# Optimization experiments

Hardware: AMD Instinct MI355X
Metric: run time of the kernel (lower is better)

Reference implementation:

```python
import jax, jax.numpy as jnp
import numpy as np

B, L, D, H = 2, 2048, 1024, 16
HD = D // H
RECENCY_BIAS = 0.1
EPS = 1e-8


def setup_inputs() -> dict:
    key = jax.random.key(0)
    k1, k2, k3, k4 = jax.random.split(key, 4)
    x = jax.random.normal(k1, (B, L, D), dtype=jnp.float32)
    # positive time gaps in [0, 10)
    time_diffs = jax.random.uniform(k2, (B, L, L), dtype=jnp.float32) * 10.0
    # packed qkv in-projection, as in nn.MultiheadAttention
    in_proj_w = jax.random.normal(k3, (3 * D, D), dtype=jnp.float32) * (D ** -0.5)
    in_proj_b = jax.random.normal(k4, (3 * D,), dtype=jnp.float32) * 0.01
    return {"x": x, "time_diffs": time_diffs, "in_proj_w": in_proj_w, "in_proj_b": in_proj_b}


def reference(x, time_diffs, in_proj_w, in_proj_b):
    # packed in-projection (q,k,v from same x, self-attention)
    qkv = x @ in_proj_w.T + in_proj_b              # [B, L, 3D]
    q, k, v = jnp.split(qkv, 3, axis=-1)
    # split heads: [B, H, L, HD]
    def heads(t):
        return t.reshape(B, L, H, HD).transpose(0, 2, 1, 3)
    q, k, v = heads(q), heads(k), heads(v)
    scores = jnp.einsum("bhqd,bhkd->bhqk", q, k) * (HD ** -0.5)
    w = jax.nn.softmax(scores, axis=-1)            # [B, H, L, L]
    # MultiheadAttention returns head-averaged weights (average_attn_weights=True)
    attn_weights = jnp.mean(w, axis=1)             # [B, L, L]
    # temporal decay reweight + renormalize
    decay = jnp.exp(-RECENCY_BIAS * time_diffs)
    attn_weights = attn_weights * decay
    attn_weights = attn_weights / (jnp.sum(attn_weights, axis=-1, keepdims=True) + EPS)
    # weighted sum against raw x (bypasses learned V / out_proj)
    output = jnp.einsum("bqk,bkd->bqd", attn_weights, x)
    return output, attn_weights
```

## Files before the change

### kernel.cpp

```cpp
#include <hip/hip_runtime.h>
#include <hip/hip_bf16.h>
#include <math.h>

namespace {
constexpr int kB = 2;
constexpr int kL = 2048;
constexpr int kD = 1024;
constexpr int kH = 16;
constexpr int kHD = 64;
constexpr float kScale = 0.125f;
constexpr float kRecency = 0.1f;
constexpr float kEps = 1e-8f;

constexpr size_t kN4 = 4194304;
}

typedef __bf16 bf16x8 __attribute__((ext_vector_type(8)));
typedef float f32x4 __attribute__((ext_vector_type(4)));
typedef unsigned short u16;
typedef u16 u16x8 __attribute__((ext_vector_type(8)));

__device__ inline u16 f2bf(float v) {
  unsigned int u = __float_as_uint(v);
  unsigned int r = (u + 0x7FFFu + ((u >> 16) & 1u)) >> 16;
  return (u16)r;
}
__device__ inline float bf2f(u16 u) { return __uint_as_float((unsigned int)u << 16); }

__global__ __launch_bounds__(256) void k_cvt_xw(const float* __restrict__ x,
                                                const float* __restrict__ w,
                                                u16* __restrict__ xh, u16* __restrict__ xl,
                                                u16* __restrict__ wh, u16* __restrict__ wl) {
  const size_t id = (size_t)blockIdx.x * 256 + threadIdx.x;
  const bool isx = id < 1048576;
  const float4 v = isx ? reinterpret_cast<const float4*>(x)[id]
                       : reinterpret_cast<const float4*>(w)[id - 1048576];
  const float vv[4] = {v.x, v.y, v.z, v.w};
  ushort4 h4, l4;
#pragma unroll
  for (int c = 0; c < 4; ++c) {
    const u16 hu = f2bf(vv[c]);
    ((u16*)&h4)[c] = hu;
    ((u16*)&l4)[c] = f2bf(vv[c] - bf2f(hu));
  }
  const size_t o = (isx ? id : id - 1048576) * 4;
  if (isx) {
    *reinterpret_cast<ushort4*>(xh + o) = h4;
    *reinterpret_cast<ushort4*>(xl + o) = l4;
  } else {
    *reinterpret_cast<ushort4*>(wh + o) = h4;
    *reinterpret_cast<ushort4*>(wl + o) = l4;
  }
}

__global__ __launch_bounds__(256, 2) void k_qkproj(const u16* __restrict__ xh, const u16* __restrict__ xl,
                                                   const u16* __restrict__ wh, const u16* __restrict__ wl,
                                                   const float* __restrict__ bias,
                                                   u16* __restrict__ qhi, u16* __restrict__ qlo,
                                                   u16* __restrict__ khi, u16* __restrict__ klo) {
  __shared__ u16 Ah[8192], Al[8192], Bh[8192], Bl[8192];
  const int tid = threadIdx.x;
  const int wave = tid >> 6, lane = tid & 63;
  const int wr = wave >> 1, wc = wave & 1;
  const int n0 = blockIdx.x * 128;
  const int m0 = blockIdx.y * 128;
  f32x4 acc[4][4] = {};
  for (int k0 = 0; k0 < kD; k0 += 64) {
    __syncthreads();
#pragma unroll
    for (int c2 = 0; c2 < 4; ++c2) {
      const int chunk = tid + c2 * 256;
      const int idx = chunk >> 3, cc = chunk & 7;
      const int lo = (((idx >> 4) * 8 + cc) * 16 + (idx & 15)) * 8;
      const size_t gw = (size_t)(n0 + idx) * kD + k0 + cc * 8;
      const size_t gx = (size_t)(m0 + idx) * kD + k0 + cc * 8;
      *reinterpret_cast<u16x8*>(&Ah[lo]) = *reinterpret_cast<const u16x8*>(wh + gw);
      *reinterpret_cast<u16x8*>(&Al[lo]) = *reinterpret_cast<const u16x8*>(wl + gw);
      *reinterpret_cast<u16x8*>(&Bh[lo]) = *reinterpret_cast<const u16x8*>(xh + gx);
      *reinterpret_cast<u16x8*>(&Bl[lo]) = *reinterpret_cast<const u16x8*>(xl + gx);
    }
    __syncthreads();
#pragma unroll
    for (int w = 0; w < 2; ++w) {
      const int kc = w * 4 + (lane >> 4);
      bf16x8 Afh[4], Afl[4], Bfh[4], Bfl[4];
#pragma unroll
      for (int i = 0; i < 4; ++i) {
        const int la = (((wr * 4 + i) * 8 + kc) * 16 + (lane & 15)) * 8;
        const int lb = (((wc * 4 + i) * 8 + kc) * 16 + (lane & 15)) * 8;
        Afh[i] = *reinterpret_cast<const bf16x8*>(&Ah[la]);
        Afl[i] = *reinterpret_cast<const bf16x8*>(&Al[la]);
        Bfh[i] = *reinterpret_cast<const bf16x8*>(&Bh[lb]);
        Bfl[i] = *reinterpret_cast<const bf16x8*>(&Bl[lb]);
      }
#pragma unroll
      for (int i = 0; i < 4; ++i)
#pragma unroll
        for (int j = 0; j < 4; ++j) {
          acc[i][j] = __builtin_amdgcn_mfma_f32_16x16x32_bf16(Afh[i], Bfh[j], acc[i][j], 0, 0, 0);
          acc[i][j] = __builtin_amdgcn_mfma_f32_16x16x32_bf16(Afh[i], Bfl[j], acc[i][j], 0, 0, 0);
          acc[i][j] = __builtin_amdgcn_mfma_f32_16x16x32_bf16(Afl[i], Bfh[j], acc[i][j], 0, 0, 0);
        }
    }
  }
  const int hglob = (n0 + wr * 64) >> 6;
  const bool isq = hglob < 16;
  const int hh = hglob & 15;
  u16* __restrict__ dh = isq ? qhi : khi;
  u16* __restrict__ dl = isq ? qlo : klo;
#pragma unroll
  for (int i = 0; i < 4; ++i) {
    const int hd0 = i * 16 + ((lane >> 4) << 2);
    const f32x4 b4 = *reinterpret_cast<const f32x4*>(bias + n0 + wr * 64 + hd0);
#pragma unroll
    for (int j = 0; j < 4; ++j) {
      const int m = m0 + wc * 64 + j * 16 + (lane & 15);
      const int bb = m >> 11, ll = m & (kL - 1);
      ushort4 vh, vl;
#pragma unroll
      for (int r = 0; r < 4; ++r) {
        const float v = acc[i][j][r] + b4[r];
        const u16 hu = f2bf(v);
        ((u16*)&vh)[r] = hu;
        ((u16*)&vl)[r] = f2bf(v - bf2f(hu));
      }
      const size_t o = (((size_t)bb * kH + hh) * kL + ll) * kHD + hd0;
      *reinterpret_cast<ushort4*>(dh + o) = vh;
      *reinterpret_cast<ushort4*>(dl + o) = vl;
    }
  }
}

__global__ __launch_bounds__(256) void k_stats(const u16* __restrict__ qh, const u16* __restrict__ ql,
                                               const u16* __restrict__ kh, const u16* __restrict__ kl,
                                               float* __restrict__ mo, float* __restrict__ ilo) {
  __shared__ u16 Kh[4096];
  __shared__ u16 Kl[4096];
  const int tid = threadIdx.x;
  const int wave = tid >> 6, lane = tid & 63;
  const int qt = blockIdx.x;
  const int bh = blockIdx.y;
  const size_t base = (size_t)bh * kL * kHD;
  const int row0 = qt * 64 + wave * 16;
  const size_t qoff = base + (size_t)(row0 + (lane & 15)) * kHD + (lane >> 4) * 8;
  const bf16x8 aqh0 = *reinterpret_cast<const bf16x8*>(qh + qoff);
  const bf16x8 aqh1 = *reinterpret_cast<const bf16x8*>(qh + qoff + 32);
  const bf16x8 aql0 = *reinterpret_cast<const bf16x8*>(ql + qoff);
  const bf16x8 aql1 = *reinterpret_cast<const bf16x8*>(ql + qoff + 32);
  float m[4], l[4];
#pragma unroll
  for (int r = 0; r < 4; ++r) { m[r] = -INFINITY; l[r] = 0.f; }
  for (int kt = 0; kt < kL; kt += 64) {
    __syncthreads();
#pragma unroll
    for (int c = tid; c < 512; c += 256) {
      const int col = c >> 3, cc = c & 7;
      const size_t g = base + (size_t)(kt + col) * kHD + cc * 8;
      const int lo = ((((col >> 4) * 2 + (cc >> 2)) * 4 + (cc & 3)) * 16 + (col & 15)) * 8;
      *reinterpret_cast<u16x8*>(&Kh[lo]) = *reinterpret_cast<const u16x8*>(kh + g);
      *reinterpret_cast<u16x8*>(&Kl[lo]) = *reinterpret_cast<const u16x8*>(kl + g);
    }
    __syncthreads();
#pragma unroll
    for (int cs = 0; cs < 4; ++cs) {
      const int f0 = (((cs * 2 + 0) * 4 + (lane >> 4)) * 16 + (lane & 15)) * 8;
      const int f1 = (((cs * 2 + 1) * 4 + (lane >> 4)) * 16 + (lane & 15)) * 8;
      const bf16x8 bh0 = *reinterpret_cast<const bf16x8*>(&Kh[f0]);
      const bf16x8 bh1 = *reinterpret_cast<const bf16x8*>(&Kh[f1]);
      const bf16x8 bl0 = *reinterpret_cast<const bf16x8*>(&Kl[f0]);
      const bf16x8 bl1 = *reinterpret_cast<const bf16x8*>(&Kl[f1]);
      f32x4 s = {0.f, 0.f, 0.f, 0.f};
      s = __builtin_amdgcn_mfma_f32_16x16x32_bf16(aqh0, bh0, s, 0, 0, 0);
      s = __builtin_amdgcn_mfma_f32_16x16x32_bf16(aqh1, bh1, s, 0, 0, 0);
      s = __builtin_amdgcn_mfma_f32_16x16x32_bf16(aqh0, bl0, s, 0, 0, 0);
      s = __builtin_amdgcn_mfma_f32_16x16x32_bf16(aqh1, bl1, s, 0, 0, 0);
      s = __builtin_amdgcn_mfma_f32_16x16x32_bf16(aql0, bh0, s, 0, 0, 0);
      s = __builtin_amdgcn_mfma_f32_16x16x32_bf16(aql1, bh1, s, 0, 0, 0);
#pragma unroll
      for (int r = 0; r < 4; ++r) {
        const float sc = s[r] * kScale;
        const float nm = fmaxf(m[r], sc);
        l[r] = l[r] * __expf(m[r] - nm) + __expf(sc - nm);
        m[r] = nm;
      }
    }
  }
#pragma unroll
  for (int r = 0; r < 4; ++r) {
#pragma unroll
    for (int off = 1; off < 16; off <<= 1) {
      const float mo2 = __shfl_xor(m[r], off);
      const float lo2 = __shfl_xor(l[r], off);
      const float nm = fmaxf(m[r], mo2);
      l[r] = l[r] * __expf(m[r] - nm) + lo2 * __expf(mo2 - nm);
      m[r] = nm;
    }
  }
  if ((lane & 15) == 0) {
#pragma unroll
    for (int r = 0; r < 4; ++r) {
      const int row = row0 + (lane >> 4) * 4 + r;
      mo[(size_t)bh * kL + row] = m[r];
      ilo[(size_t)bh * kL + row] = 1.0f / l[r];
    }
  }
}

__global__ __launch_bounds__(256) void k_attn(const u16* __restrict__ qh, const u16* __restrict__ ql,
                                              const u16* __restrict__ kh, const u16* __restrict__ kl,
                                              const float* __restrict__ ms, const float* __restrict__ ils,
                                              const float* __restrict__ td,
                                              float* __restrict__ attn, float* __restrict__ rowsum) {
  __shared__ u16 Kh[8192];
  __shared__ u16 Kl[8192];
  __shared__ float msS[16][64];
  __shared__ float ilS[16][64];
  const int tid = threadIdx.x;
  const int wave = tid >> 6, lane = tid & 63;
  const int kb = blockIdx.x;
  const int qb = blockIdx.y;
  const int b = blockIdx.z;
#pragma unroll
  for (int c = tid; c < 1024; c += 256) {
    const int h = c >> 6, r = c & 63;
    msS[h][r] = ms[((size_t)b * kH + h) * kL + qb * 64 + r];
    ilS[h][r] = ils[((size_t)b * kH + h) * kL + qb * 64 + r];
  }
  const int row0 = qb * 64 + wave * 16;
  float wacc[8][4] = {};
  for (int h = 0; h < kH; ++h) {
    const size_t base = ((size_t)b * kH + h) * kL * kHD;
    __syncthreads();
#pragma unroll
    for (int c = tid; c < 1024; c += 256) {
      const int col = c >> 3, cc = c & 7;
      const size_t g = base + (size_t)(kb * 128 + col) * kHD + cc * 8;
      const int lo = ((((col >> 4) * 2 + (cc >> 2)) * 4 + (cc & 3)) * 16 + (col & 15)) * 8;
      *reinterpret_cast<u16x8*>(&Kh[lo]) = *reinterpret_cast<const u16x8*>(kh + g);
      *reinterpret_cast<u16x8*>(&Kl[lo]) = *reinterpret_cast<const u16x8*>(kl + g);
    }
    __syncthreads();
    const size_t qoff = base + (size_t)(row0 + (lane & 15)) * kHD + (lane >> 4) * 8;
    const bf16x8 aqh0 = *reinterpret_cast<const bf16x8*>(qh + qoff);
    const bf16x8 aqh1 = *reinterpret_cast<const bf16x8*>(qh + qoff + 32);
    const bf16x8 aql0 = *reinterpret_cast<const bf16x8*>(ql + qoff);
    const bf16x8 aql1 = *reinterpret_cast<const bf16x8*>(ql + qoff + 32);
    const f32x4 mrow = *reinterpret_cast<const f32x4*>(&msS[h][wave * 16 + (lane >> 4) * 4]);
    const f32x4 irow = *reinterpret_cast<const f32x4*>(&ilS[h][wave * 16 + (lane >> 4) * 4]);
#pragma unroll
    for (int cs = 0; cs < 8; ++cs) {
      const int f0 = (((cs * 2 + 0) * 4 + (lane >> 4)) * 16 + (lane & 15)) * 8;
      const int f1 = (((cs * 2 + 1) * 4 + (lane >> 4)) * 16 + (lane & 15)) * 8;
      const bf16x8 bkh0 = *reinterpret_cast<const bf16x8*>(&Kh[f0]);
      const bf16x8 bkh1 = *reinterpret_cast<const bf16x8*>(&Kh[f1]);
      const bf16x8 bkl0 = *reinterpret_cast<const bf16x8*>(&Kl[f0]);
      const bf16x8 bkl1 = *reinterpret_cast<const bf16x8*>(&Kl[f1]);
      f32x4 s = {0.f, 0.f, 0.f, 0.f};
      s = __builtin_amdgcn_mfma_f32_16x16x32_bf16(aqh0, bkh0, s, 0, 0, 0);
      s = __builtin_amdgcn_mfma_f32_16x16x32_bf16(aqh1, bkh1, s, 0, 0, 0);
      s = __builtin_amdgcn_mfma_f32_16x16x32_bf16(aqh0, bkl0, s, 0, 0, 0);
      s = __builtin_amdgcn_mfma_f32_16x16x32_bf16(aqh1, bkl1, s, 0, 0, 0);
      s = __builtin_amdgcn_mfma_f32_16x16x32_bf16(aql0, bkh0, s, 0, 0, 0);
      s = __builtin_amdgcn_mfma_f32_16x16x32_bf16(aql1, bkh1, s, 0, 0, 0);
#pragma unroll
      for (int r = 0; r < 4; ++r)
        wacc[cs][r] += __expf(fmaf(s[r], kScale, -mrow[r])) * irow[r];
    }
  }
  const float invH = 1.0f / kH;
#pragma unroll
  for (int r = 0; r < 4; ++r) {
    const int row = row0 + (lane >> 4) * 4 + r;
    float rs = 0.f;
#pragma unroll
    for (int cs = 0; cs < 8; ++cs) {
      const int col = kb * 128 + cs * 16 + (lane & 15);
      const size_t idx = ((size_t)b * kL + row) * kL + col;
      const float o = wacc[cs][r] * invH * __expf(-kRecency * td[idx]);
      attn[idx] = o;
      rs += o;
    }
#pragma unroll
    for (int off = 1; off < 16; off <<= 1) rs += __shfl_xor(rs, off);
    if ((lane & 15) == 0) atomicAdd(&rowsum[(size_t)b * kL + row], rs);
  }
}

__global__ __launch_bounds__(256) void k_norm(float* __restrict__ attn,
                                              const float* __restrict__ rowsum,
                                              u16* __restrict__ abf) {
  const int row = blockIdx.x;
  const float inv = 1.0f / (rowsum[row] + kEps);
  float* p = attn + (size_t)row * kL;
  u16* q = abf + (size_t)row * kL;
  const int i0 = threadIdx.x * 8;
  float4 a = *reinterpret_cast<float4*>(p + i0);
  float4 b = *reinterpret_cast<float4*>(p + i0 + 4);
  a.x *= inv; a.y *= inv; a.z *= inv; a.w *= inv;
  b.x *= inv; b.y *= inv; b.z *= inv; b.w *= inv;
  *reinterpret_cast<float4*>(p + i0) = a;
  *reinterpret_cast<float4*>(p + i0 + 4) = b;
  u16x8 h;
  h[0] = f2bf(a.x); h[1] = f2bf(a.y); h[2] = f2bf(a.z); h[3] = f2bf(a.w);
  h[4] = f2bf(b.x); h[5] = f2bf(b.y); h[6] = f2bf(b.z); h[7] = f2bf(b.w);
  *reinterpret_cast<u16x8*>(q + i0) = h;
}

__global__ __launch_bounds__(256) void k_cvt_xT(const float* __restrict__ x,
                                                u16* __restrict__ xth, u16* __restrict__ xtl) {
  __shared__ u16 Th[64][72];
  __shared__ u16 Tl[64][72];
  const int tid = threadIdx.x;
  const int l0 = blockIdx.x * 64, d0 = blockIdx.y * 64, b = blockIdx.z;
#pragma unroll
  for (int rep = 0; rep < 4; ++rep) {
    const int lr = (tid >> 4) + rep * 16;
    const int dc = (tid & 15) * 4;
    const float4 v = *reinterpret_cast<const float4*>(x + ((size_t)b * kL + l0 + lr) * kD + d0 + dc);
    const float vv[4] = {v.x, v.y, v.z, v.w};
#pragma unroll
    for (int c = 0; c < 4; ++c) {
      const u16 hu = f2bf(vv[c]);
      Th[dc + c][lr] = hu;
      Tl[dc + c][lr] = f2bf(vv[c] - bf2f(hu));
    }
  }
  __syncthreads();
#pragma unroll
  for (int rep = 0; rep < 2; ++rep) {
    const int chunk = tid + rep * 256;
    const int dd = chunk >> 3, part = chunk & 7;
    const size_t o = ((size_t)b * kD + d0 + dd) * kL + l0 + part * 8;
    *reinterpret_cast<u16x8*>(xth + o) = *reinterpret_cast<const u16x8*>(&Th[dd][part * 8]);
    *reinterpret_cast<u16x8*>(xtl + o) = *reinterpret_cast<const u16x8*>(&Tl[dd][part * 8]);
  }
}

__global__ __launch_bounds__(256, 2) void k_out(const u16* __restrict__ abf,
                                                const u16* __restrict__ xth, const u16* __restrict__ xtl,
                                                float* __restrict__ out) {
  __shared__ u16 Ah[8192], Bh[8192], Bl[8192];
  const int tid = threadIdx.x;
  const int wave = tid >> 6, lane = tid & 63;
  const int wr = wave >> 1, wc = wave & 1;
  const int m0 = blockIdx.x * 128;
  const int n0 = blockIdx.y * 128;
  const int b = blockIdx.z;
  f32x4 acc[4][4] = {};
  for (int k0 = 0; k0 < kL; k0 += 64) {
    __syncthreads();
#pragma unroll
    for (int c2 = 0; c2 < 4; ++c2) {
      const int chunk = tid + c2 * 256;
      const int idx = chunk >> 3, cc = chunk & 7;
      const int lo = (((idx >> 4) * 8 + cc) * 16 + (idx & 15)) * 8;
      const size_t ga = ((size_t)b * kL + m0 + idx) * kL + k0 + cc * 8;
      const size_t gb = ((size_t)b * kD + n0 + idx) * kL + k0 + cc * 8;
      *reinterpret_cast<u16x8*>(&Ah[lo]) = *reinterpret_cast<const u16x8*>(abf + ga);
      *reinterpret_cast<u16x8*>(&Bh[lo]) = *reinterpret_cast<const u16x8*>(xth + gb);
      *reinterpret_cast<u16x8*>(&Bl[lo]) = *reinterpret_cast<const u16x8*>(xtl + gb);
    }
    __syncthreads();
#pragma unroll
    for (int w = 0; w < 2; ++w) {
      const int kc = w * 4 + (lane >> 4);
      bf16x8 Afh[4], Bfh[4], Bfl[4];
#pragma unroll
      for (int i = 0; i < 4; ++i) {
        const int la = (((wr * 4 + i) * 8 + kc) * 16 + (lane & 15)) * 8;
        const int lb = (((wc * 4 + i) * 8 + kc) * 16 + (lane & 15)) * 8;
        Afh[i] = *reinterpret_cast<const bf16x8*>(&Ah[la]);
        Bfh[i] = *reinterpret_cast<const bf16x8*>(&Bh[lb]);
        Bfl[i] = *reinterpret_cast<const bf16x8*>(&Bl[lb]);
      }
#pragma unroll
      for (int i = 0; i < 4; ++i)
#pragma unroll
        for (int j = 0; j < 4; ++j) {
          acc[i][j] = __builtin_amdgcn_mfma_f32_16x16x32_bf16(Afh[i], Bfh[j], acc[i][j], 0, 0, 0);
          acc[i][j] = __builtin_amdgcn_mfma_f32_16x16x32_bf16(Afh[i], Bfl[j], acc[i][j], 0, 0, 0);
        }
    }
  }
#pragma unroll
  for (int i = 0; i < 4; ++i) {
    const int row = m0 + wr * 64 + i * 16 + ((lane >> 4) << 2);
#pragma unroll
    for (int j = 0; j < 4; ++j) {
      const int col = n0 + wc * 64 + j * 16 + (lane & 15);
#pragma unroll
      for (int r = 0; r < 4; ++r)
        out[((size_t)b * kL + row + r) * kD + col] = acc[i][j][r];
    }
  }
}

extern "C" void kernel_launch(void* const* d_in, const int* in_sizes, int n_in,
                              void* d_out, int out_size, void* d_ws, size_t ws_size,
                              hipStream_t stream) {
  (void)in_sizes; (void)n_in; (void)out_size; (void)ws_size;
  const float* x = (const float*)d_in[0];
  const float* td = (const float*)d_in[1];
  const float* w = (const float*)d_in[2];
  const float* bias = (const float*)d_in[3];
  float* out = (float*)d_out;
  float* attn = out + (size_t)kB * kL * kD;

  u16* base = (u16*)d_ws;
  u16* qhi = base;
  u16* qlo = base + kN4;
  u16* khi = base + 2 * kN4;
  u16* klo = base + 3 * kN4;
  u16* xah = base + 4 * kN4;
  u16* xal = base + 5 * kN4;
  u16* attn_bf = xah;
  u16* xth = qhi;
  u16* xtl = qlo;
  u16* whi = base + 6 * kN4;
  u16* wlo = whi + 2097152;
  float* fb = (float*)(wlo + 2097152);
  float* mb = fb;
  float* ilb = fb + 65536;
  float* rsb = fb + 131072;

  hipLaunchKernelGGL(k_cvt_xw, dim3(6144), dim3(256), 0, stream, x, w, xah, xal, whi, wlo);
  hipLaunchKernelGGL(k_qkproj, dim3(16, 32), dim3(256), 0, stream, xah, xal, whi, wlo, bias,
                     qhi, qlo, khi, klo);
  hipLaunchKernelGGL(k_stats, dim3(32, 32), dim3(256), 0, stream, qhi, qlo, khi, klo, mb, ilb);
  hipMemsetAsync(rsb, 0, (size_t)kB * kL * sizeof(float), stream);
  hipLaunchKernelGGL(k_attn, dim3(16, 32, 2), dim3(256), 0, stream, qhi, qlo, khi, klo, mb, ilb,
                     td, attn, rsb);
  hipLaunchKernelGGL(k_norm, dim3(kB * kL), dim3(256), 0, stream, attn, rsb, attn_bf);
  hipLaunchKernelGGL(k_cvt_xT, dim3(32, 16, 2), dim3(256), 0, stream, x, xth, xtl);
  hipLaunchKernelGGL(k_out, dim3(16, 8, 2), dim3(256), 0, stream, attn_bf, xth, xtl, out);
}
```

Before: 507.1 us.

## Switch split-precision MFMA from bf16 to fp16 and drop online max in softmax stats

Replaces bf16 hi/lo split arithmetic with fp16, which has more mantissa bits, so fewer correction MFMAs are needed: two instead of three in the projection, and four instead of six in the score GEMMs. The x low part and the K low part are no longer produced at all. Q is prescaled by scale*log2e so softmax can use exp2, and the online max is dropped: the stats kernel sums exp2 directly, with a fixed -4 offset folding in the head average, and the attn kernel uses one log-normalizer. LDS layouts get a padded stride to reduce bank conflicts, and the stats kernel reads K straight from global memory. Without the max subtraction, exp2 can overflow or lose accuracy if scores are large, and fp16 range limits may affect accuracy.

```diff
diff --git a/kernel.cpp b/kernel.cpp
--- a/kernel.cpp
+++ b/kernel.cpp
@@ -8,57 +8,50 @@
 constexpr int kD = 1024;
 constexpr int kH = 16;
 constexpr int kHD = 64;
-constexpr float kScale = 0.125f;
-constexpr float kRecency = 0.1f;
+constexpr float kQScale = 0.125f * 1.44269504088896340736f;
+constexpr float kDecay2 = -0.1f * 1.44269504088896340736f;
 constexpr float kEps = 1e-8f;
-
 constexpr size_t kN4 = 4194304;
 }
 
-typedef __bf16 bf16x8 __attribute__((ext_vector_type(8)));
+typedef _Float16 f16;
+typedef f16 f16x4 __attribute__((ext_vector_type(4)));
+typedef f16 f16x8 __attribute__((ext_vector_type(8)));
 typedef float f32x4 __attribute__((ext_vector_type(4)));
-typedef unsigned short u16;
-typedef u16 u16x8 __attribute__((ext_vector_type(8)));
-
-__device__ inline u16 f2bf(float v) {
-  unsigned int u = __float_as_uint(v);
-  unsigned int r = (u + 0x7FFFu + ((u >> 16) & 1u)) >> 16;
-  return (u16)r;
-}
-__device__ inline float bf2f(u16 u) { return __uint_as_float((unsigned int)u << 16); }
 
 __global__ __launch_bounds__(256) void k_cvt_xw(const float* __restrict__ x,
                                                 const float* __restrict__ w,
-                                                u16* __restrict__ xh, u16* __restrict__ xl,
-                                                u16* __restrict__ wh, u16* __restrict__ wl) {
+                                                f16* __restrict__ xh,
+                                                f16* __restrict__ wh, f16* __restrict__ wl) {
   const size_t id = (size_t)blockIdx.x * 256 + threadIdx.x;
-  const bool isx = id < 1048576;
-  const float4 v = isx ? reinterpret_cast<const float4*>(x)[id]
-                       : reinterpret_cast<const float4*>(w)[id - 1048576];
-  const float vv[4] = {v.x, v.y, v.z, v.w};
-  ushort4 h4, l4;
-#pragma unroll
-  for (int c = 0; c < 4; ++c) {
-    const u16 hu = f2bf(vv[c]);
-    ((u16*)&h4)[c] = hu;
-    ((u16*)&l4)[c] = f2bf(vv[c] - bf2f(hu));
-  }
-  const size_t o = (isx ? id : id - 1048576) * 4;
-  if (isx) {
-    *reinterpret_cast<ushort4*>(xh + o) = h4;
-    *reinterpret_cast<ushort4*>(xl + o) = l4;
+  if (id < 1048576) {
+    const float4 v = reinterpret_cast<const float4*>(x)[id];
+    const float vv[4] = {v.x, v.y, v.z, v.w};
+    f16x4 h;
+#pragma unroll
+    for (int c = 0; c < 4; ++c) h[c] = (f16)vv[c];
+    *reinterpret_cast<f16x4*>(xh + id * 4) = h;
   } else {
-    *reinterpret_cast<ushort4*>(wh + o) = h4;
-    *reinterpret_cast<ushort4*>(wl + o) = l4;
-  }
-}
-
-__global__ __launch_bounds__(256, 2) void k_qkproj(const u16* __restrict__ xh, const u16* __restrict__ xl,
-                                                   const u16* __restrict__ wh, const u16* __restrict__ wl,
+    const size_t id2 = id - 1048576;
+    const float4 v = reinterpret_cast<const float4*>(w)[id2];
+    const float vv[4] = {v.x, v.y, v.z, v.w};
+    f16x4 h, l;
+#pragma unroll
+    for (int c = 0; c < 4; ++c) {
+      h[c] = (f16)vv[c];
+      l[c] = (f16)(vv[c] - (float)h[c]);
+    }
+    *reinterpret_cast<f16x4*>(wh + id2 * 4) = h;
+    *reinterpret_cast<f16x4*>(wl + id2 * 4) = l;
+  }
+}
+
+__global__ __launch_bounds__(256, 2) void k_qkproj(const f16* __restrict__ xh,
+                                                   const f16* __restrict__ wh, const f16* __restrict__ wl,
                                                    const float* __restrict__ bias,
-                                                   u16* __restrict__ qhi, u16* __restrict__ qlo,
-                                                   u16* __restrict__ khi, u16* __restrict__ klo) {
-  __shared__ u16 Ah[8192], Al[8192], Bh[8192], Bl[8192];
+                                                   f16* __restrict__ qhi, f16* __restrict__ qlo,
+                                                   f16* __restrict__ khi) {
+  __shared__ f16 Ah[8704], Al[8704], Bh[8704];
   const int tid = threadIdx.x;
   const int wave = tid >> 6, lane = tid & 63;
   const int wr = wave >> 1, wc = wave & 1;
@@ -71,43 +64,38 @@
     for (int c2 = 0; c2 < 4; ++c2) {
       const int chunk = tid + c2 * 256;
       const int idx = chunk >> 3, cc = chunk & 7;
-      const int lo = (((idx >> 4) * 8 + cc) * 16 + (idx & 15)) * 8;
+      const int lo = ((idx >> 4) * 8 + cc) * 136 + (idx & 15) * 8;
       const size_t gw = (size_t)(n0 + idx) * kD + k0 + cc * 8;
       const size_t gx = (size_t)(m0 + idx) * kD + k0 + cc * 8;
-      *reinterpret_cast<u16x8*>(&Ah[lo]) = *reinterpret_cast<const u16x8*>(wh + gw);
-      *reinterpret_cast<u16x8*>(&Al[lo]) = *reinterpret_cast<const u16x8*>(wl + gw);
-      *reinterpret_cast<u16x8*>(&Bh[lo]) = *reinterpret_cast<const u16x8*>(xh + gx);
-      *reinterpret_cast<u16x8*>(&Bl[lo]) = *reinterpret_cast<const u16x8*>(xl + gx);
-    }
-    __syncthreads();
-#pragma unroll
-    for (int w = 0; w < 2; ++w) {
-      const int kc = w * 4 + (lane >> 4);
-      bf16x8 Afh[4], Afl[4], Bfh[4], Bfl[4];
+      *reinterpret_cast<f16x8*>(&Ah[lo]) = *reinterpret_cast<const f16x8*>(wh + gw);
+      *reinterpret_cast<f16x8*>(&Al[lo]) = *reinterpret_cast<const f16x8*>(wl + gw);
+      *reinterpret_cast<f16x8*>(&Bh[lo]) = *reinterpret_cast<const f16x8*>(xh + gx);
+    }
+    __syncthreads();
+#pragma unroll
+    for (int z = 0; z < 2; ++z) {
+      const int kc = z * 4 + (lane >> 4);
+      f16x8 Afh[4], Afl[4], Bfh[4];
 #pragma unroll
       for (int i = 0; i < 4; ++i) {
-        const int la = (((wr * 4 + i) * 8 + kc) * 16 + (lane & 15)) * 8;
-        const int lb = (((wc * 4 + i) * 8 + kc) * 16 + (lane & 15)) * 8;
-        Afh[i] = *reinterpret_cast<const bf16x8*>(&Ah[la]);
-        Afl[i] = *reinterpret_cast<const bf16x8*>(&Al[la]);
-        Bfh[i] = *reinterpret_cast<const bf16x8*>(&Bh[lb]);
-        Bfl[i] = *reinterpret_cast<const bf16x8*>(&Bl[lb]);
+        const int la = ((wr * 4 + i) * 8 + kc) * 136 + (lane & 15) * 8;
+        const int lb = ((wc * 4 + i) * 8 + kc) * 136 + (lane & 15) * 8;
+        Afh[i] = *reinterpret_cast<const f16x8*>(&Ah[la]);
+        Afl[i] = *reinterpret_cast<const f16x8*>(&Al[la]);
+        Bfh[i] = *reinterpret_cast<const f16x8*>(&Bh[lb]);
       }
 #pragma unroll
       for (int i = 0; i < 4; ++i)
 #pragma unroll
         for (int j = 0; j < 4; ++j) {
-          acc[i][j] = __builtin_amdgcn_mfma_f32_16x16x32_bf16(Afh[i], Bfh[j], acc[i][j], 0, 0, 0);
-          acc[i][j] = __builtin_amdgcn_mfma_f32_16x16x32_bf16(Afh[i], Bfl[j], acc[i][j], 0, 0, 0);
-          acc[i][j] = __builtin_amdgcn_mfma_f32_16x16x32_bf16(Afl[i], Bfh[j], acc[i][j], 0, 0, 0);
+          acc[i][j] = __builtin_amdgcn_mfma_f32_16x16x32_f16(Afh[i], Bfh[j], acc[i][j], 0, 0, 0);
+          acc[i][j] = __builtin_amdgcn_mfma_f32_16x16x32_f16(Afl[i], Bfh[j], acc[i][j], 0, 0, 0);
         }
     }
   }
   const int hglob = (n0 + wr * 64) >> 6;
   const bool isq = hglob < 16;
   const int hh = hglob & 15;
-  u16* __restrict__ dh = isq ? qhi : khi;
-  u16* __restrict__ dl = isq ? qlo : klo;
 #pragma unroll
   for (int i = 0; i < 4; ++i) {
     const int hd0 = i * 16 + ((lane >> 4) << 2);
@@ -116,26 +104,30 @@
     for (int j = 0; j < 4; ++j) {
       const int m = m0 + wc * 64 + j * 16 + (lane & 15);
       const int bb = m >> 11, ll = m & (kL - 1);
-      ushort4 vh, vl;
-#pragma unroll
-      for (int r = 0; r < 4; ++r) {
-        const float v = acc[i][j][r] + b4[r];
-        const u16 hu = f2bf(v);
-        ((u16*)&vh)[r] = hu;
-        ((u16*)&vl)[r] = f2bf(v - bf2f(hu));
+      const size_t o = (((size_t)bb * kH + hh) * kL + ll) * kHD + hd0;
+      if (isq) {
+        f16x4 vh, vl;
+#pragma unroll
+        for (int r = 0; r < 4; ++r) {
+          const float v = (acc[i][j][r] + b4[r]) * kQScale;
+          vh[r] = (f16)v;
+          vl[r] = (f16)(v - (float)vh[r]);
+        }
+        *reinterpret_cast<f16x4*>(qhi + o) = vh;
+        *reinterpret_cast<f16x4*>(qlo + o) = vl;
+      } else {
+        f16x4 vh;
+#pragma unroll
+        for (int r = 0; r < 4; ++r) vh[r] = (f16)(acc[i][j][r] + b4[r]);
+        *reinterpret_cast<f16x4*>(khi + o) = vh;
       }
-      const size_t o = (((size_t)bb * kH + hh) * kL + ll) * kHD + hd0;
-      *reinterpret_cast<ushort4*>(dh + o) = vh;
-      *reinterpret_cast<ushort4*>(dl + o) = vl;
-    }
-  }
-}
-
-__global__ __launch_bounds__(256) void k_stats(const u16* __restrict__ qh, const u16* __restrict__ ql,
-                                               const u16* __restrict__ kh, const u16* __restrict__ kl,
-                                               float* __restrict__ mo, float* __restrict__ ilo) {
-  __shared__ u16 Kh[4096];
-  __shared__ u16 Kl[4096];
+    }
+  }
+}
+
+__global__ __launch_bounds__(256) void k_stats(const f16* __restrict__ qh, const f16* __restrict__ ql,
+                                               const f16* __restrict__ kh,
+                                               float* __restrict__ nlo) {
   const int tid = threadIdx.x;
   const int wave = tid >> 6, lane = tid & 63;
   const int qt = blockIdx.x;
@@ -143,131 +135,86 @@
   const size_t base = (size_t)bh * kL * kHD;
   const int row0 = qt * 64 + wave * 16;
   const size_t qoff = base + (size_t)(row0 + (lane & 15)) * kHD + (lane >> 4) * 8;
-  const bf16x8 aqh0 = *reinterpret_cast<const bf16x8*>(qh + qoff);
-  const bf16x8 aqh1 = *reinterpret_cast<const bf16x8*>(qh + qoff + 32);
-  const bf16x8 aql0 = *reinterpret_cast<const bf16x8*>(ql + qoff);
-  const bf16x8 aql1 = *reinterpret_cast<const bf16x8*>(ql + qoff + 32);
-  float m[4], l[4];
-#pragma unroll
-  for (int r = 0; r < 4; ++r) { m[r] = -INFINITY; l[r] = 0.f; }
-  for (int kt = 0; kt < kL; kt += 64) {
-    __syncthreads();
-#pragma unroll
-    for (int c = tid; c < 512; c += 256) {
-      const int col = c >> 3, cc = c & 7;
-      const size_t g = base + (size_t)(kt + col) * kHD + cc * 8;
-      const int lo = ((((col >> 4) * 2 + (cc >> 2)) * 4 + (cc & 3)) * 16 + (col & 15)) * 8;
-      *reinterpret_cast<u16x8*>(&Kh[lo]) = *reinterpret_cast<const u16x8*>(kh + g);
-      *reinterpret_cast<u16x8*>(&Kl[lo]) = *reinterpret_cast<const u16x8*>(kl + g);
-    }
-    __syncthreads();
-#pragma unroll
-    for (int cs = 0; cs < 4; ++cs) {
-      const int f0 = (((cs * 2 + 0) * 4 + (lane >> 4)) * 16 + (lane & 15)) * 8;
-      const int f1 = (((cs * 2 + 1) * 4 + (lane >> 4)) * 16 + (lane & 15)) * 8;
-      const bf16x8 bh0 = *reinterpret_cast<const bf16x8*>(&Kh[f0]);
-      const bf16x8 bh1 = *reinterpret_cast<const bf16x8*>(&Kh[f1]);
-      const bf16x8 bl0 = *reinterpret_cast<const bf16x8*>(&Kl[f0]);
-      const bf16x8 bl1 = *reinterpret_cast<const bf16x8*>(&Kl[f1]);
-      f32x4 s = {0.f, 0.f, 0.f, 0.f};
-      s = __builtin_amdgcn_mfma_f32_16x16x32_bf16(aqh0, bh0, s, 0, 0, 0);
-      s = __builtin_amdgcn_mfma_f32_16x16x32_bf16(aqh1, bh1, s, 0, 0, 0);
-      s = __builtin_amdgcn_mfma_f32_16x16x32_bf16(aqh0, bl0, s, 0, 0, 0);
-      s = __builtin_amdgcn_mfma_f32_16x16x32_bf16(aqh1, bl1, s, 0, 0, 0);
-      s = __builtin_amdgcn_mfma_f32_16x16x32_bf16(aql0, bh0, s, 0, 0, 0);
-      s = __builtin_amdgcn_mfma_f32_16x16x32_bf16(aql1, bh1, s, 0, 0, 0);
-#pragma unroll
-      for (int r = 0; r < 4; ++r) {
-        const float sc = s[r] * kScale;
-        const float nm = fmaxf(m[r], sc);
-        l[r] = l[r] * __expf(m[r] - nm) + __expf(sc - nm);
-        m[r] = nm;
-      }
-    }
+  const f16x8 aqh0 = *reinterpret_cast<const f16x8*>(qh + qoff);
+  const f16x8 aqh1 = *reinterpret_cast<const f16x8*>(qh + qoff + 32);
+  const f16x8 aql0 = *reinterpret_cast<const f16x8*>(ql + qoff);
+  const f16x8 aql1 = *reinterpret_cast<const f16x8*>(ql + qoff + 32);
+  const f16* kp = kh + base + ((lane & 15) << 6) + ((lane >> 4) << 3);
+  float l[4] = {0.f, 0.f, 0.f, 0.f};
+#pragma unroll 8
+  for (int kt = 0; kt < kL; kt += 16) {
+    const f16* p = kp + (size_t)kt * kHD;
+    const f16x8 b0 = *reinterpret_cast<const f16x8*>(p);
+    const f16x8 b1 = *reinterpret_cast<const f16x8*>(p + 32);
+    f32x4 s = {0.f, 0.f, 0.f, 0.f};
+    s = __builtin_amdgcn_mfma_f32_16x16x32_f16(aqh0, b0, s, 0, 0, 0);
+    s = __builtin_amdgcn_mfma_f32_16x16x32_f16(aql0, b0, s, 0, 0, 0);
+    s = __builtin_amdgcn_mfma_f32_16x16x32_f16(aqh1, b1, s, 0, 0, 0);
+    s = __builtin_amdgcn_mfma_f32_16x16x32_f16(aql1, b1, s, 0, 0, 0);
+#pragma unroll
+    for (int r = 0; r < 4; ++r) l[r] += exp2f(s[r]);
   }
 #pragma unroll
   for (int r = 0; r < 4; ++r) {
 #pragma unroll
-    for (int off = 1; off < 16; off <<= 1) {
-      const float mo2 = __shfl_xor(m[r], off);
-      const float lo2 = __shfl_xor(l[r], off);
-      const float nm = fmaxf(m[r], mo2);
-      l[r] = l[r] * __expf(m[r] - nm) + lo2 * __expf(mo2 - nm);
-      m[r] = nm;
-    }
+    for (int off = 1; off < 16; off <<= 1) l[r] += __shfl_xor(l[r], off);
   }
   if ((lane & 15) == 0) {
 #pragma unroll
-    for (int r = 0; r < 4; ++r) {
-      const int row = row0 + (lane >> 4) * 4 + r;
-      mo[(size_t)bh * kL + row] = m[r];
-      ilo[(size_t)bh * kL + row] = 1.0f / l[r];
-    }
-  }
-}
-
-__global__ __launch_bounds__(256) void k_attn(const u16* __restrict__ qh, const u16* __restrict__ ql,
-                                              const u16* __restrict__ kh, const u16* __restrict__ kl,
-                                              const float* __restrict__ ms, const float* __restrict__ ils,
+    for (int r = 0; r < 4; ++r)
+      nlo[(size_t)bh * kL + row0 + (lane >> 4) * 4 + r] = -log2f(l[r]) - 4.0f;
+  }
+}
+
+__global__ __launch_bounds__(256) void k_attn(const f16* __restrict__ qh, const f16* __restrict__ ql,
+                                              const f16* __restrict__ kh,
+                                              const float* __restrict__ nl,
                                               const float* __restrict__ td,
                                               float* __restrict__ attn, float* __restrict__ rowsum) {
-  __shared__ u16 Kh[8192];
-  __shared__ u16 Kl[8192];
-  __shared__ float msS[16][64];
-  __shared__ float ilS[16][64];
+  __shared__ f16 Kh[8704];
+  __shared__ float nlS[16][64];
   const int tid = threadIdx.x;
   const int wave = tid >> 6, lane = tid & 63;
   const int kb = blockIdx.x;
   const int qb = blockIdx.y;
   const int b = blockIdx.z;
 #pragma unroll
-  for (int c = tid; c < 1024; c += 256) {
-    const int h = c >> 6, r = c & 63;
-    msS[h][r] = ms[((size_t)b * kH + h) * kL + qb * 64 + r];
-    ilS[h][r] = ils[((size_t)b * kH + h) * kL + qb * 64 + r];
-  }
+  for (int c = tid; c < 1024; c += 256)
+    nlS[c >> 6][c & 63] = nl[((size_t)b * kH + (c >> 6)) * kL + qb * 64 + (c & 63)];
   const int row0 = qb * 64 + wave * 16;
   float wacc[8][4] = {};
   for (int h = 0; h < kH; ++h) {
     const size_t base = ((size_t)b * kH + h) * kL * kHD;
-    __syncthreads();
-#pragma unroll
-    for (int c = tid; c < 1024; c += 256) {
-      const int col = c >> 3, cc = c & 7;
-      const size_t g = base + (size_t)(kb * 128 + col) * kHD + cc * 8;
-      const int lo = ((((col >> 4) * 2 + (cc >> 2)) * 4 + (cc & 3)) * 16 + (col & 15)) * 8;
-      *reinterpret_cast<u16x8*>(&Kh[lo]) = *reinterpret_cast<const u16x8*>(kh + g);
-      *reinterpret_cast<u16x8*>(&Kl[lo]) = *reinterpret_cast<const u16x8*>(kl + g);
-    }
-    __syncthreads();
     const size_t qoff = base + (size_t)(row0 + (lane & 15)) * kHD + (lane >> 4) * 8;
-    const bf16x8 aqh0 = *reinterpret_cast<const bf16x8*>(qh + qoff);
-    const bf16x8 aqh1 = *reinterpret_cast<const bf16x8*>(qh + qoff + 32);
-    const bf16x8 aql0 = *reinterpret_cast<const bf16x8*>(ql + qoff);
-    const bf16x8 aql1 = *reinterpret_cast<const bf16x8*>(ql + qoff + 32);
-    const f32x4 mrow = *reinterpret_cast<const f32x4*>(&msS[h][wave * 16 + (lane >> 4) * 4]);
-    const f32x4 irow = *reinterpret_cast<const f32x4*>(&ilS[h][wave * 16 + (lane >> 4) * 4]);
+    const f16x8 aqh0 = *reinterpret_cast<const f16x8*>(qh + qoff);
+    const f16x8 aqh1 = *reinterpret_cast<const f16x8*>(qh + qoff + 32);
+    const f16x8 aql0 = *reinterpret_cast<const f16x8*>(ql + qoff);
+    const f16x8 aql1 = *reinterpret_cast<const f16x8*>(ql + qoff + 32);
+    __syncthreads();
+#pragma unroll
+    for (int c2 = 0; c2 < 4; ++c2) {
+      const int chunk = tid + c2 * 256;
+      const int col = chunk >> 3, cc = chunk & 7;
+      const int lo = ((col >> 4) * 8 + cc) * 136 + (col & 15) * 8;
+      *reinterpret_cast<f16x8*>(&Kh[lo]) =
+          *reinterpret_cast<const f16x8*>(kh + base + (size_t)(kb * 128 + col) * kHD + cc * 8);
+    }
+    __syncthreads();
+    const f32x4 nlr = *reinterpret_cast<const f32x4*>(&nlS[h][wave * 16 + (lane >> 4) * 4]);
 #pragma unroll
     for (int cs = 0; cs < 8; ++cs) {
-      const int f0 = (((cs * 2 + 0) * 4 + (lane >> 4)) * 16 + (lane & 15)) * 8;
-      const int f1 = (((cs * 2 + 1) * 4 + (lane >> 4)) * 16 + (lane & 15)) * 8;
-      const bf16x8 bkh0 = *reinterpret_cast<const bf16x8*>(&Kh[f0]);
-      const bf16x8 bkh1 = *reinterpret_cast<const bf16x8*>(&Kh[f1]);
-      const bf16x8 bkl0 = *reinterpret_cast<const bf16x8*>(&Kl[f0]);
-      const bf16x8 bkl1 = *reinterpret_cast<const bf16x8*>(&Kl[f1]);
+      const int r0 = (cs * 8 + (lane >> 4)) * 136 + (lane & 15) * 8;
+      const f16x8 b0 = *reinterpret_cast<const f16x8*>(&Kh[r0]);
+      const f16x8 b1 = *reinterpret_cast<const f16x8*>(&Kh[r0 + 4 * 136]);
       f32x4 s = {0.f, 0.f, 0.f, 0.f};
-      s = __builtin_amdgcn_mfma_f32_16x16x32_bf16(aqh0, bkh0, s, 0, 0, 0);
-      s = __builtin_amdgcn_mfma_f32_16x16x32_bf16(aqh1, bkh1, s, 0, 0, 0);
-      s = __builtin_amdgcn_mfma_f32_16x16x32_bf16(aqh0, bkl0, s, 0, 0, 0);
-      s = __builtin_amdgcn_mfma_f32_16x16x32_bf16(aqh1, bkl1, s, 0, 0, 0);
-      s = __builtin_amdgcn_mfma_f32_16x16x32_bf16(aql0, bkh0, s, 0, 0, 0);
-      s = __builtin_amdgcn_mfma_f32_16x16x32_bf16(aql1, bkh1, s, 0, 0, 0);
-#pragma unroll
-      for (int r = 0; r < 4; ++r)
-        wacc[cs][r] += __expf(fmaf(s[r], kScale, -mrow[r])) * irow[r];
-    }
-  }
-  const float invH = 1.0f / kH;
+      s = __builtin_amdgcn_mfma_f32_16x16x32_f16(aqh0, b0, s, 0, 0, 0);
+      s = __builtin_amdgcn_mfma_f32_16x16x32_f16(aql0, b0, s, 0, 0, 0);
+      s = __builtin_amdgcn_mfma_f32_16x16x32_f16(aqh1, b1, s, 0, 0, 0);
+      s = __builtin_amdgcn_mfma_f32_16x16x32_f16(aql1, b1, s, 0, 0, 0);
+#pragma unroll
+      for (int r = 0; r < 4; ++r) wacc[cs][r] += exp2f(s[r] + nlr[r]);
+    }
+  }
 #pragma unroll
   for (int r = 0; r < 4; ++r) {
     const int row = row0 + (lane >> 4) * 4 + r;
@@ -276,7 +223,7 @@
     for (int cs = 0; cs < 8; ++cs) {
       const int col = kb * 128 + cs * 16 + (lane & 15);
       const size_t idx = ((size_t)b * kL + row) * kL + col;
-      const float o = wacc[cs][r] * invH * __expf(-kRecency * td[idx]);
+      const float o = wacc[cs][r] * exp2f(kDecay2 * td[idx]);
       attn[idx] = o;
       rs += o;
     }
@@ -288,11 +235,11 @@
 
 __global__ __launch_bounds__(256) void k_norm(float* __restrict__ attn,
                                               const float* __restrict__ rowsum,
-                                              u16* __restrict__ abf) {
+                                              f16* __restrict__ abf) {
   const int row = blockIdx.x;
   const float inv = 1.0f / (rowsum[row] + kEps);
   float* p = attn + (size_t)row * kL;
-  u16* q = abf + (size_t)row * kL;
+  f16* q = abf + (size_t)row * kL;
   const int i0 = threadIdx.x * 8;
   float4 a = *reinterpret_cast<float4*>(p + i0);
   float4 b = *reinterpret_cast<float4*>(p + i0 + 4);
@@ -300,16 +247,16 @@
   b.x *= inv; b.y *= inv; b.z *= inv; b.w *= inv;
   *reinterpret_cast<float4*>(p + i0) = a;
   *reinterpret_cast<float4*>(p + i0 + 4) = b;
-  u16x8 h;
-  h[0] = f2bf(a.x); h[1] = f2bf(a.y); h[2] = f2bf(a.z); h[3] = f2bf(a.w);
-  h[4] = f2bf(b.x); h[5] = f2bf(b.y); h[6] = f2bf(b.z); h[7] = f2bf(b.w);
-  *reinterpret_cast<u16x8*>(q + i0) = h;
+  f16x8 h;
+  h[0] = (f16)a.x; h[1] = (f16)a.y; h[2] = (f16)a.z; h[3] = (f16)a.w;
+  h[4] = (f16)b.x; h[5] = (f16)b.y; h[6] = (f16)b.z; h[7] = (f16)b.w;
+  *reinterpret_cast<f16x8*>(q + i0) = h;
 }
 
 __global__ __launch_bounds__(256) void k_cvt_xT(const float* __restrict__ x,
-                                                u16* __restrict__ xth, u16* __restrict__ xtl) {
-  __shared__ u16 Th[64][72];
-  __shared__ u16 Tl[64][72];
+                                                f16* __restrict__ xth, f16* __restrict__ xtl) {
+  __shared__ f16 Th[64][72];
+  __shared__ f16 Tl[64][72];
   const int tid = threadIdx.x;
   const int l0 = blockIdx.x * 64, d0 = blockIdx.y * 64, b = blockIdx.z;
 #pragma unroll
@@ -320,9 +267,9 @@
     const float vv[4] = {v.x, v.y, v.z, v.w};
 #pragma unroll
     for (int c = 0; c < 4; ++c) {
-      const u16 hu = f2bf(vv[c]);
+      const f16 hu = (f16)vv[c];
       Th[dc + c][lr] = hu;
-      Tl[dc + c][lr] = f2bf(vv[c] - bf2f(hu));
+      Tl[dc + c][lr] = (f16)(vv[c] - (float)hu);
     }
   }
   __syncthreads();
@@ -331,15 +278,15 @@
     const int chunk = tid + rep * 256;
     const int dd = chunk >> 3, part = chunk & 7;
     const size_t o = ((size_t)b * kD + d0 + dd) * kL + l0 + part * 8;
-    *reinterpret_cast<u16x8*>(xth + o) = *reinterpret_cast<const u16x8*>(&Th[dd][part * 8]);
-    *reinterpret_cast<u16x8*>(xtl + o) = *reinterpret_cast<const u16x8*>(&Tl[dd][part * 8]);
-  }
-}
-
-__global__ __launch_bounds__(256, 2) void k_out(const u16* __restrict__ abf,
-                                                const u16* __restrict__ xth, const u16* __restrict__ xtl,
+    *reinterpret_cast<f16x8*>(xth + o) = *reinterpret_cast<const f16x8*>(&Th[dd][part * 8]);
+    *reinterpret_cast<f16x8*>(xtl + o) = *reinterpret_cast<const f16x8*>(&Tl[dd][part * 8]);
+  }
+}
+
+__global__ __launch_bounds__(256, 2) void k_out(const f16* __restrict__ abf,
+                                                const f16* __restrict__ xth, const f16* __restrict__ xtl,
                                                 float* __restrict__ out) {
-  __shared__ u16 Ah[8192], Bh[8192], Bl[8192];
+  __shared__ f16 Ah[8704], Bh[8704], Bl[8704];
   const int tid = threadIdx.x;
   const int wave = tid >> 6, lane = tid & 63;
   const int wr = wave >> 1, wc = wave & 1;
@@ -353,32 +300,32 @@
     for (int c2 = 0; c2 < 4; ++c2) {
       const int chunk = tid + c2 * 256;
       const int idx = chunk >> 3, cc = chunk & 7;
-      const int lo = (((idx >> 4) * 8 + cc) * 16 + (idx & 15)) * 8;
+      const int lo = ((idx >> 4) * 8 + cc) * 136 + (idx & 15) * 8;
       const size_t ga = ((size_t)b * kL + m0 + idx) * kL + k0 + cc * 8;
       const size_t gb = ((size_t)b * kD + n0 + idx) * kL + k0 + cc * 8;
-      *reinterpret_cast<u16x8*>(&Ah[lo]) = *reinterpret_cast<const u16x8*>(abf + ga);
-      *reinterpret_cast<u16x8*>(&Bh[lo]) = *reinterpret_cast<const u16x8*>(xth + gb);
-      *reinterpret_cast<u16x8*>(&Bl[lo]) = *reinterpret_cast<const u16x8*>(xtl + gb);
-    }
-    __syncthreads();
-#pragma unroll
-    for (int w = 0; w < 2; ++w) {
-      const int kc = w * 4 + (lane >> 4);
-      bf16x8 Afh[4], Bfh[4], Bfl[4];
+      *reinterpret_cast<f16x8*>(&Ah[lo]) = *reinterpret_cast<const f16x8*>(abf + ga);
+      *reinterpret_cast<f16x8*>(&Bh[lo]) = *reinterpret_cast<const f16x8*>(xth + gb);
+      *reinterpret_cast<f16x8*>(&Bl[lo]) = *reinterpret_cast<const f16x8*>(xtl + gb);
+    }
+    __syncthreads();
+#pragma unroll
+    for (int z = 0; z < 2; ++z) {
+      const int kc = z * 4 + (lane >> 4);
+      f16x8 Afh[4], Bfh[4], Bfl[4];
 #pragma unroll
       for (int i = 0; i < 4; ++i) {
-        const int la = (((wr * 4 + i) * 8 + kc) * 16 + (lane & 15)) * 8;
-        const int lb = (((wc * 4 + i) * 8 + kc) * 16 + (lane & 15)) * 8;
-        Afh[i] = *reinterpret_cast<const bf16x8*>(&Ah[la]);
-        Bfh[i] = *reinterpret_cast<const bf16x8*>(&Bh[lb]);
-        Bfl[i] = *reinterpret_cast<const bf16x8*>(&Bl[lb]);
+        const int la = ((wr * 4 + i) * 8 + kc) * 136 + (lane & 15) * 8;
+        const int lb = ((wc * 4 + i) * 8 + kc) * 136 + (lane & 15) * 8;
+        Afh[i] = *reinterpret_cast<const f16x8*>(&Ah[la]);
+        Bfh[i] = *reinterpret_cast<const f16x8*>(&Bh[lb]);
+        Bfl[i] = *reinterpret_cast<const f16x8*>(&Bl[lb]);
       }
 #pragma unroll
       for (int i = 0; i < 4; ++i)
 #pragma unroll
         for (int j = 0; j < 4; ++j) {
-          acc[i][j] = __builtin_amdgcn_mfma_f32_16x16x32_bf16(Afh[i], Bfh[j], acc[i][j], 0, 0, 0);
-          acc[i][j] = __builtin_amdgcn_mfma_f32_16x16x32_bf16(Afh[i], Bfl[j], acc[i][j], 0, 0, 0);
+          acc[i][j] = __builtin_amdgcn_mfma_f32_16x16x32_f16(Afh[i], Bfh[j], acc[i][j], 0, 0, 0);
+          acc[i][j] = __builtin_amdgcn_mfma_f32_16x16x32_f16(Afh[i], Bfl[j], acc[i][j], 0, 0, 0);
         }
     }
   }
@@ -406,31 +353,26 @@
   float* out = (float*)d_out;
   float* attn = out + (size_t)kB * kL * kD;
 
-  u16* base = (u16*)d_ws;
-  u16* qhi = base;
-  u16* qlo = base + kN4;
-  u16* khi = base + 2 * kN4;
-  u16* klo = base + 3 * kN4;
-  u16* xah = base + 4 * kN4;
-  u16* xal = base + 5 * kN4;
-  u16* attn_bf = xah;
-  u16* xth = qhi;
-  u16* xtl = qlo;
-  u16* whi = base + 6 * kN4;
-  u16* wlo = whi + 2097152;
-  float* fb = (float*)(wlo + 2097152);
-  float* mb = fb;
-  float* ilb = fb + 65536;
-  float* rsb = fb + 131072;
-
-  hipLaunchKernelGGL(k_cvt_xw, dim3(6144), dim3(256), 0, stream, x, w, xah, xal, whi, wlo);
-  hipLaunchKernelGGL(k_qkproj, dim3(16, 32), dim3(256), 0, stream, xah, xal, whi, wlo, bias,
-                     qhi, qlo, khi, klo);
-  hipLaunchKernelGGL(k_stats, dim3(32, 32), dim3(256), 0, stream, qhi, qlo, khi, klo, mb, ilb);
+  f16* base = (f16*)d_ws;
+  f16* qh = base;
+  f16* ql = base + kN4;
+  f16* kh = base + 2 * kN4;
+  f16* xh = base + 3 * kN4;
+  f16* wh = base + 4 * kN4;
+  f16* wl = wh + 2097152;
+  f16* attn_f16 = xh;
+  f16* xth = qh;
+  f16* xtl = ql;
+  float* fb = (float*)(wl + 2097152);
+  float* nl = fb;
+  float* rsb = fb + 65536;
+
+  hipLaunchKernelGGL(k_cvt_xw, dim3(6144), dim3(256), 0, stream, x, w, xh, wh, wl);
+  hipLaunchKernelGGL(k_qkproj, dim3(16, 32), dim3(256), 0, stream, xh, wh, wl, bias, qh, ql, kh);
+  hipLaunchKernelGGL(k_stats, dim3(32, 32), dim3(256), 0, stream, qh, ql, kh, nl);
   hipMemsetAsync(rsb, 0, (size_t)kB * kL * sizeof(float), stream);
-  hipLaunchKernelGGL(k_attn, dim3(16, 32, 2), dim3(256), 0, stream, qhi, qlo, khi, klo, mb, ilb,
-                     td, attn, rsb);
-  hipLaunchKernelGGL(k_norm, dim3(kB * kL), dim3(256), 0, stream, attn, rsb, attn_bf);
+  hipLaunchKernelGGL(k_attn, dim3(16, 32, 2), dim3(256), 0, stream, qh, ql, kh, nl, td, attn, rsb);
+  hipLaunchKernelGGL(k_norm, dim3(kB * kL), dim3(256), 0, stream, attn, rsb, attn_f16);
   hipLaunchKernelGGL(k_cvt_xT, dim3(32, 16, 2), dim3(256), 0, stream, x, xth, xtl);
-  hipLaunchKernelGGL(k_out, dim3(16, 8, 2), dim3(256), 0, stream, attn_bf, xth, xtl, out);
-}
+  hipLaunchKernelGGL(k_out, dim3(16, 8, 2), dim3(256), 0, stream, attn_f16, xth, xtl, out);
+}
```

Result: faster. 407.1 us (-19.7%).
